# Kernel tuning notes

Measured on AMD Instinct MI355X. Metric: run time of the kernel, lower is better.

The kernel has to match this reference:

```python
import jax, jax.numpy as jnp
import numpy as np
from functools import partial

K = 1024
EMA_DECAY = 0.99
TOL = 1e-4
EPS = 1e-5
MAX_ITERS = 10


def setup_inputs() -> dict:
    key = jax.random.key(0)
    x = jax.random.normal(key, (32, 256, 1024), dtype=jnp.float32)
    return {"x": x}


def _sq_dists(xf, x_sq, centers):
    # squared euclidean distances [N, K]; argmin is identical to torch.cdist argmin
    c_sq = jnp.sum(centers * centers, axis=1)
    return x_sq[:, None] + c_sq[None, :] - 2.0 * (xf @ centers.T)


def reference(x):
    b, c, t = x.shape
    xf = jnp.transpose(x, (0, 2, 1)).reshape(-1, c)  # [N, c], N = b*t
    N = xf.shape[0]
    # _init_centers: random permutation of rows, take first K (training mode)
    perm = jax.random.permutation(jax.random.key(1), N)[:K]
    ema0 = xf[perm]  # [K, c]
    x_sq = jnp.sum(xf * xf, axis=1)  # [N]
    ones = jnp.ones((N,), dtype=xf.dtype)

    def step(carry, _):
        ema, labels_prev, done = carry
        d = _sq_dists(xf, x_sq, ema)
        labels = jnp.argmin(d, axis=1)  # [N]
        counts = jax.ops.segment_sum(ones, labels, num_segments=K)  # [K]
        sums = jax.ops.segment_sum(xf, labels, num_segments=K)      # [K, c]
        centers = sums / (counts[:, None] + EPS)
        # dead-center handling: keep old ema center where cluster is empty
        centers = jnp.where((counts == 0)[:, None], ema, centers)
        new_ema = ema * EMA_DECAY + (1.0 - EMA_DECAY) * centers
        err = jnp.linalg.norm(new_ema - centers)
        # torch loop breaks AFTER the ema update of the converged iteration;
        # once done, later iterations are no-ops.
        ema_out = jnp.where(done, ema, new_ema)
        labels_out = jnp.where(done, labels_prev, labels)
        new_done = jnp.logical_or(done, err < TOL)
        return (ema_out, labels_out, new_done), None

    init = (ema0, jnp.zeros((N,), dtype=jnp.int32), jnp.array(False))
    (ema, labels, done), _ = jax.lax.scan(step, init, None, length=MAX_ITERS)

    # if loop never broke, torch recomputes labels against final ema centers
    labels_final = jnp.argmin(_sq_dists(xf, x_sq, ema), axis=1)
    return jnp.where(done, labels, labels_final)
```

## Files before the change

kernel.cpp:

```cpp
#include <hip/hip_runtime.h>
#include <stdint.h>

#define JAX_PARTITIONABLE 1

static constexpr int C_ = 256;
static constexpr int T_ = 1024;
static constexpr int N_ = 32768;
static constexpr int K_ = 1024;
static constexpr float MARGIN_ = 0.02f;

typedef __attribute__((ext_vector_type(8))) short short8;
typedef __attribute__((ext_vector_type(4))) float f32x4;

__host__ __device__ __forceinline__ void tf2x32(uint32_t k0, uint32_t k1,
                                                uint32_t x0, uint32_t x1,
                                                uint32_t& o0, uint32_t& o1) {
  const uint32_t ks2 = k0 ^ k1 ^ 0x1BD11BDAu;
  uint32_t v0 = x0 + k0, v1 = x1 + k1;
#define TFR(d) { v0 += v1; v1 = (v1 << d) | (v1 >> (32 - d)); v1 ^= v0; }
#define TF4A TFR(13) TFR(15) TFR(26) TFR(6)
#define TF4B TFR(17) TFR(29) TFR(16) TFR(24)
  TF4A v0 += k1;  v1 += ks2 + 1u;
  TF4B v0 += ks2; v1 += k0 + 2u;
  TF4A v0 += k0;  v1 += k1 + 3u;
  TF4B v0 += k1;  v1 += ks2 + 4u;
  TF4A v0 += ks2; v1 += k0 + 5u;
  o0 = v0; o1 = v1;
#undef TFR
#undef TF4A
#undef TF4B
}

__device__ __forceinline__ uint16_t f2bf(float f) {
  const uint32_t u = __float_as_uint(f);
  return (uint16_t)((u + 0x7FFFu + ((u >> 16) & 1u)) >> 16);
}
__device__ __forceinline__ float bf2f(uint16_t h) {
  return __uint_as_float(((uint32_t)h) << 16);
}

__device__ __forceinline__ void write_bfrag(uint16_t* __restrict__ bH, uint16_t* __restrict__ bL,
                                            int k, int c, float v) {
  const int kt = k >> 4;
  const int lane = (k & 15) + (((c & 31) >> 3) << 4);
  const int ck = c >> 5;
  const int j = c & 7;
  const uint16_t h = f2bf(v);
  const uint16_t l = f2bf(v - bf2f(h));
  const size_t idx = ((((size_t)(kt << 3) + ck) << 6) + lane) * 8 + j;
  bH[idx] = h; bL[idx] = l;
}

__global__ void bits_kernel(uint32_t k0, uint32_t k1, unsigned long long* __restrict__ keys) {
#if JAX_PARTITIONABLE
  const int i = blockIdx.x * 256 + threadIdx.x;
  uint32_t o0, o1; tf2x32(k0, k1, 0u, (uint32_t)i, o0, o1);
  keys[i] = (((unsigned long long)(o0 ^ o1)) << 32) | (unsigned)i;
#else
  const int j = blockIdx.x * 256 + threadIdx.x;
  uint32_t o0, o1; tf2x32(k0, k1, (uint32_t)j, (uint32_t)(j + 16384), o0, o1);
  keys[j]         = (((unsigned long long)o0) << 32) | (unsigned)j;
  keys[j + 16384] = (((unsigned long long)o1) << 32) | (unsigned)(j + 16384);
#endif
}

__global__ void bhist_kernel(const unsigned long long* __restrict__ keys, int* __restrict__ bcnt) {
  const int i = blockIdx.x * 256 + threadIdx.x;
  atomicAdd(&bcnt[(int)(keys[i] >> 56)], 1);
}

__global__ void bscan_kernel(const int* __restrict__ bcnt, int* __restrict__ boff,
                             int* __restrict__ bcur) {
  if (threadIdx.x == 0) {
    int run = 0;
    for (int i = 0; i < 256; ++i) { boff[i] = run; bcur[i] = run; run += bcnt[i]; }
    boff[256] = run;
  }
}

__global__ void bscatter_kernel(const unsigned long long* __restrict__ keys,
                                int* __restrict__ bcur, unsigned long long* __restrict__ barr) {
  const int i = blockIdx.x * 256 + threadIdx.x;
  const unsigned long long k = keys[i];
  const int pos = atomicAdd(&bcur[(int)(k >> 56)], 1);
  barr[pos] = k;
}

template<int ROUND>
__global__ void brank_kernel(const unsigned long long* __restrict__ barr,
                             const int* __restrict__ boff,
                             int* __restrict__ val1, int* __restrict__ perm) {
  const int i = blockIdx.x * 256 + threadIdx.x;
  const unsigned long long my = barr[i];
  const int b = (int)(my >> 56);
  const int lo = boff[b], hi = boff[b + 1];
  int cnt = 0;
  #pragma unroll 4
  for (int j = lo; j < hi; ++j) cnt += (barr[j] < my) ? 1 : 0;
  const int r = lo + cnt;
  const int idx = (int)(uint32_t)my;
  if (ROUND == 1) {
    val1[r] = idx;
  } else {
    if (r < K_) perm[r] = val1[idx];
  }
}

__global__ void transpose_kernel(const float* __restrict__ x, float* __restrict__ xT) {
  __shared__ float tile[256][33];
  const int tid = threadIdx.x;
  const int b = blockIdx.x >> 5, tt = blockIdx.x & 31;
  const int t0 = tt << 5;
  const float* xb = x + (size_t)b * (C_ * T_) + t0;
  #pragma unroll
  for (int i = 0; i < 32; ++i) {
    const int idx = tid + (i << 8);
    const int c = idx >> 5, p = idx & 31;
    tile[c][p] = xb[(size_t)c * T_ + p];
  }
  __syncthreads();
  float* dst = xT + (((size_t)(b << 10) + t0) << 8);
  #pragma unroll
  for (int p = 0; p < 32; ++p)
    dst[((size_t)p << 8) + tid] = tile[tid][p];
}

__device__ __forceinline__ double block_reduce_256_f64(double v, double* red) {
  #pragma unroll
  for (int s = 1; s < 64; s <<= 1) v += __shfl_xor(v, s, 64);
  if ((threadIdx.x & 63) == 0) red[threadIdx.x >> 6] = v;
  __syncthreads();
  return red[0] + red[1] + red[2] + red[3];
}

__global__ void init_ema_kernel(const float* __restrict__ x, const int* __restrict__ perm,
                                float* __restrict__ ema, uint16_t* __restrict__ bfH,
                                uint16_t* __restrict__ bfL,
                                double* __restrict__ csq, float* __restrict__ csq32) {
  __shared__ double red[4];
  const int k = blockIdx.x, c = threadIdx.x;
  const int n = perm[k];
  const int b = n >> 10, t = n & 1023;
  const float v = x[(size_t)b * (C_ * T_) + (size_t)c * T_ + t];
  ema[((size_t)k << 8) + c] = v;
  write_bfrag(bfH, bfL, k, c, v);
  const double s = block_reduce_256_f64((double)v * (double)v, red);
  if (c == 0) { csq[k] = s; csq32[k] = (float)s; }
}

__global__ void update_kernel(float* __restrict__ ema, uint16_t* __restrict__ bfH,
                              uint16_t* __restrict__ bfL,
                              const double* __restrict__ sums4, const int* __restrict__ counts,
                              double* __restrict__ csq, float* __restrict__ csq32) {
  __shared__ double red[4];
  const int k = blockIdx.x, c = threadIdx.x;
  const size_t idx = ((size_t)k << 8) + c;
  const int cnt = counts[k];
  const float e = ema[idx];
  float center;
  if (cnt == 0) {
    center = e;
  } else {
    double sd = 0.0;
    #pragma unroll
    for (int sl = 0; sl < 4; ++sl) sd += sums4[((size_t)((sl << 10) + k) << 8) + c];
    const float s32 = (float)sd;
    const float denom = __fadd_rn((float)cnt, 1e-5f);
    center = __fdiv_rn(s32, denom);
  }
  const float ne = __fadd_rn(__fmul_rn(e, 0.99f), __fmul_rn(0.01f, center));
  ema[idx] = ne;
  write_bfrag(bfH, bfL, k, c, ne);
  const double s = block_reduce_256_f64((double)ne * (double)ne, red);
  if (c == 0) { csq[k] = s; csq32[k] = (float)s; }
}

#define AF(pl, mt, ck, lane) (((((((pl) << 2) + (mt)) << 3) + (ck)) << 6) + (lane))
__global__ __launch_bounds__(256, 2) void assign_mfma(
    const float* __restrict__ x, const short8* __restrict__ bfH, const short8* __restrict__ bfL,
    const float* __restrict__ csq32, int* __restrict__ labels,
    int* __restrict__ flagidx, int* __restrict__ flagcnt) {
  __shared__ __align__(16) char smem[81920];
  short8* afrag = (short8*)smem;
  float (*xstage)[64] = (float(*)[64])(smem + 65536);
  float* mg_d = (float*)(smem + 65536);
  float* mg_2 = mg_d + 256;
  int*   mg_k = (int*)(mg_2 + 256);

  const int tid = threadIdx.x;
  const int n0 = blockIdx.x << 6;
  const int b = n0 >> 10, t0 = n0 & 1023;
  const float* xb = x + (size_t)b * (C_ * T_) + t0;

  #pragma unroll 1
  for (int q = 0; q < 4; ++q) {
    #pragma unroll
    for (int i = 0; i < 16; ++i) {
      const int idx = tid + (i << 8);
      const int c = idx >> 6, p = idx & 63;
      xstage[c][p] = xb[(size_t)((q << 6) + c) * T_ + p];
    }
    __syncthreads();
    #pragma unroll
    for (int i = 0; i < 2; ++i) {
      const int slot = tid + (i << 8);
      const int lane = slot & 63;
      const int ckh = (slot >> 6) & 1;
      const int mt = slot >> 7;
      const int row = lane & 15;
      const int kof = (lane >> 4) << 3;
      short8 h8, l8;
      #pragma unroll
      for (int j = 0; j < 8; ++j) {
        const float v = xstage[(ckh << 5) + kof + j][(mt << 4) + row];
        const uint16_t hh = f2bf(v);
        h8[j] = (short)hh;
        l8[j] = (short)f2bf(v - bf2f(hh));
      }
      const int ck = (q << 1) + ckh;
      afrag[AF(0, mt, ck, lane)] = h8;
      afrag[AF(1, mt, ck, lane)] = l8;
    }
    __syncthreads();
  }

  const int w = tid >> 6, lane = tid & 63;

  float bd[16], b2[16]; int bk[16];
  #pragma unroll
  for (int s = 0; s < 16; ++s) { bd[s] = 3.0e38f; b2[s] = 3.0e38f; bk[s] = 0; }

  const short8* afH = afrag;
  const short8* afL = afrag + 2048;

  #pragma unroll 1
  for (int g = 0; g < 4; ++g) {
    f32x4 acc[4][4];
    #pragma unroll
    for (int mt = 0; mt < 4; ++mt)
      #pragma unroll
      for (int t = 0; t < 4; ++t) acc[mt][t] = (f32x4){0.f, 0.f, 0.f, 0.f};

    #pragma unroll 1
    for (int pass = 0; pass < 3; ++pass) {
      const short8* ap = (pass == 2) ? afL : afH;
      const short8* bp = (pass == 1) ? bfL : bfH;
      #pragma unroll 2
      for (int ck = 0; ck < 8; ++ck) {
        short8 a0 = ap[(0 << 9) + (ck << 6) + lane];
        short8 a1 = ap[(1 << 9) + (ck << 6) + lane];
        short8 a2 = ap[(2 << 9) + (ck << 6) + lane];
        short8 a3 = ap[(3 << 9) + (ck << 6) + lane];
        const size_t bbase = ((((size_t)(w << 4) + (g << 2)) << 3) + ck) * 64 + lane;
        #pragma unroll
        for (int t = 0; t < 4; ++t) {
          const short8 bf = bp[bbase + (size_t)t * 512];
          acc[0][t] = __builtin_amdgcn_mfma_f32_16x16x32_bf16(a0, bf, acc[0][t], 0, 0, 0);
          acc[1][t] = __builtin_amdgcn_mfma_f32_16x16x32_bf16(a1, bf, acc[1][t], 0, 0, 0);
          acc[2][t] = __builtin_amdgcn_mfma_f32_16x16x32_bf16(a2, bf, acc[2][t], 0, 0, 0);
          acc[3][t] = __builtin_amdgcn_mfma_f32_16x16x32_bf16(a3, bf, acc[3][t], 0, 0, 0);
        }
      }
    }
    #pragma unroll
    for (int t = 0; t < 4; ++t) {
      const int kt = (w << 4) + (g << 2) + t;
      const int k = (kt << 4) + (lane & 15);
      const float cq = csq32[k];
      #pragma unroll
      for (int mt = 0; mt < 4; ++mt)
        #pragma unroll
        for (int r = 0; r < 4; ++r) {
          const float d = cq - 2.0f * acc[mt][t][r];
          const int s = (mt << 2) + r;
          if (d < bd[s]) { b2[s] = bd[s]; bd[s] = d; bk[s] = k; }
          else if (d < b2[s]) b2[s] = d;
        }
    }
  }

  #pragma unroll
  for (int s = 0; s < 16; ++s) {
    #pragma unroll
    for (int sh = 1; sh < 16; sh <<= 1) {
      const float od = __shfl_xor(bd[s], sh, 64);
      const float o2 = __shfl_xor(b2[s], sh, 64);
      const int   ok = __shfl_xor(bk[s], sh, 64);
      if (od < bd[s] || (od == bd[s] && ok < bk[s])) {
        b2[s] = fminf(o2, bd[s]); bd[s] = od; bk[s] = ok;
      } else {
        b2[s] = fminf(b2[s], od);
      }
    }
  }
  if ((lane & 15) == 0) {
    #pragma unroll
    for (int s = 0; s < 16; ++s) {
      const int mt = s >> 2, r = s & 3;
      const int pt = (mt << 4) + ((lane >> 4) << 2) + r;
      mg_d[(w << 6) + pt] = bd[s]; mg_2[(w << 6) + pt] = b2[s]; mg_k[(w << 6) + pt] = bk[s];
    }
  }
  __syncthreads();

  if (tid < 64) {
    float fb = mg_d[tid], f2 = mg_2[tid]; int fk = mg_k[tid];
    #pragma unroll
    for (int ww = 1; ww < 4; ++ww) {
      const float od = mg_d[(ww << 6) + tid], o2 = mg_2[(ww << 6) + tid];
      const int ok = mg_k[(ww << 6) + tid];
      if (od < fb) { f2 = fminf(fb, o2); fb = od; fk = ok; }
      else f2 = fminf(f2, fminf(od, o2));
    }
    const int n = n0 + tid;
    labels[n] = fk;
    if (f2 - fb <= MARGIN_) { const int p = atomicAdd(flagcnt, 1); flagidx[p] = n; }
  }
}

__global__ void refine_kernel(const float* __restrict__ x, const float* __restrict__ ema,
                              const double* __restrict__ csq,
                              const int* __restrict__ flagidx, const int* __restrict__ flagcnt,
                              int* __restrict__ labels) {
  __shared__ float xr[C_];
  __shared__ double rd[4]; __shared__ int rk[4];
  const int tid = threadIdx.x;
  const int cnt = *flagcnt;
  for (int it = blockIdx.x; it < cnt; it += gridDim.x) {
    const int n = flagidx[it];
    const int b = n >> 10, t = n & 1023;
    xr[tid] = x[(size_t)b * (C_ * T_) + (size_t)tid * T_ + t];
    __syncthreads();
    double bdv = 1e300; int bkv = 0;
    #pragma unroll 1
    for (int r = 0; r < 4; ++r) {
      const int k = (r << 8) + tid;
      const float* er = ema + ((size_t)k << 8);
      double acc = 0.0;
      #pragma unroll 4
      for (int c4 = 0; c4 < 64; ++c4) {
        const float4 ev = *(const float4*)(er + (c4 << 2));
        const float4 xv = *(const float4*)(&xr[c4 << 2]);
        acc = fma((double)xv.x, (double)ev.x, acc);
        acc = fma((double)xv.y, (double)ev.y, acc);
        acc = fma((double)xv.z, (double)ev.z, acc);
        acc = fma((double)xv.w, (double)ev.w, acc);
      }
      const double d = csq[k] - 2.0 * acc;
      if (d < bdv) { bdv = d; bkv = k; }
    }
    #pragma unroll
    for (int s = 1; s < 64; s <<= 1) {
      const double od = __shfl_xor(bdv, s, 64);
      const int    ok = __shfl_xor(bkv, s, 64);
      if (od < bdv || (od == bdv && ok < bkv)) { bdv = od; bkv = ok; }
    }
    if ((tid & 63) == 0) { rd[tid >> 6] = bdv; rk[tid >> 6] = bkv; }
    __syncthreads();
    if (tid == 0) {
      #pragma unroll
      for (int wv = 1; wv < 4; ++wv)
        if (rd[wv] < bdv || (rd[wv] == bdv && rk[wv] < bkv)) { bdv = rd[wv]; bkv = rk[wv]; }
      if (bkv != labels[n]) labels[n] = bkv;
    }
    __syncthreads();
  }
}

__global__ void hist_kernel(const int* __restrict__ labels, int* __restrict__ counts) {
  const int n = blockIdx.x * 256 + threadIdx.x;
  atomicAdd(&counts[labels[n]], 1);
}

__global__ void prefix_kernel(const int* __restrict__ counts, int* __restrict__ offsets,
                              int* __restrict__ cursor) {
  __shared__ int wsum[4];
  const int tid = threadIdx.x;
  const int lane = tid & 63, w = tid >> 6;
  const int c0 = counts[(tid << 2)], c1 = counts[(tid << 2) + 1];
  const int c2 = counts[(tid << 2) + 2], c3 = counts[(tid << 2) + 3];
  const int s = c0 + c1 + c2 + c3;
  int inc = s;
  #pragma unroll
  for (int sh = 1; sh < 64; sh <<= 1) {
    const int t = __shfl_up(inc, sh, 64);
    if (lane >= sh) inc += t;
  }
  if (lane == 63) wsum[w] = inc;
  __syncthreads();
  int wof = 0;
  #pragma unroll
  for (int i = 0; i < 4; ++i) if (i < w) wof += wsum[i];
  int run = wof + inc - s;
  offsets[(tid << 2)] = run;     cursor[(tid << 2)] = run;     run += c0;
  offsets[(tid << 2) + 1] = run; cursor[(tid << 2) + 1] = run; run += c1;
  offsets[(tid << 2) + 2] = run; cursor[(tid << 2) + 2] = run; run += c2;
  offsets[(tid << 2) + 3] = run; cursor[(tid << 2) + 3] = run;
}

__global__ void scatter_sorted_kernel(const int* __restrict__ labels, int* __restrict__ cursor,
                                      int* __restrict__ sortedIdx) {
  const int n = blockIdx.x * 256 + threadIdx.x;
  const int pos = atomicAdd(&cursor[labels[n]], 1);
  sortedIdx[pos] = n;
}

template<int TRANS>
__global__ void segsum_kernel(const float* __restrict__ x, const float* __restrict__ xT,
                              const int* __restrict__ sortedIdx, const int* __restrict__ offsets,
                              const int* __restrict__ counts, double* __restrict__ sums4) {
  const int k = blockIdx.x >> 2, sl = blockIdx.x & 3;
  const int tid = threadIdx.x;
  const int cnt = counts[k], off = offsets[k];
  const int i0 = (cnt * sl) >> 2, i1 = (cnt * (sl + 1)) >> 2;
  double acc = 0.0;
  int i = i0;
  for (; i + 4 <= i1; i += 4) {
    float v0, v1, v2, v3;
    if (TRANS) {
      const int na = sortedIdx[off + i],     nb = sortedIdx[off + i + 1];
      const int nc = sortedIdx[off + i + 2], nd = sortedIdx[off + i + 3];
      v0 = xT[((size_t)na << 8) + tid]; v1 = xT[((size_t)nb << 8) + tid];
      v2 = xT[((size_t)nc << 8) + tid]; v3 = xT[((size_t)nd << 8) + tid];
    } else {
      const int na = sortedIdx[off + i],     nb = sortedIdx[off + i + 1];
      const int nc = sortedIdx[off + i + 2], nd = sortedIdx[off + i + 3];
      v0 = x[(size_t)(na >> 10) * (C_ * T_) + (size_t)tid * T_ + (na & 1023)];
      v1 = x[(size_t)(nb >> 10) * (C_ * T_) + (size_t)tid * T_ + (nb & 1023)];
      v2 = x[(size_t)(nc >> 10) * (C_ * T_) + (size_t)tid * T_ + (nc & 1023)];
      v3 = x[(size_t)(nd >> 10) * (C_ * T_) + (size_t)tid * T_ + (nd & 1023)];
    }
    acc += (double)v0; acc += (double)v1; acc += (double)v2; acc += (double)v3;
  }
  for (; i < i1; ++i) {
    const int n = sortedIdx[off + i];
    const float v = TRANS ? xT[((size_t)n << 8) + tid]
                          : x[(size_t)(n >> 10) * (C_ * T_) + (size_t)tid * T_ + (n & 1023)];
    acc += (double)v;
  }
  sums4[((size_t)((sl << 10) + k) << 8) + tid] = acc;
}

extern "C" void kernel_launch(void* const* d_in, const int* in_sizes, int n_in,
                              void* d_out, int out_size, void* d_ws, size_t ws_size,
                              hipStream_t stream) {
  const float* x = (const float*)d_in[0];
  int* out = (int*)d_out;
  char* ws = (char*)d_ws;

  float*    ema   = (float*)   (ws + 0);
  uint16_t* bfH   = (uint16_t*)(ws + 1048576);
  uint16_t* bfL   = (uint16_t*)(ws + 1572864);
  double*   sums4 = (double*)  (ws + 2097152);
  unsigned long long* keys = (unsigned long long*)(ws + 2097152);
  unsigned long long* barr = (unsigned long long*)(ws + 2097152 + 262144);
  int*    val1   = (int*)  (ws + 2097152 + 524288);
  const size_t MISC = 2097152 + 8388608;
  int*    counts  = (int*)  (ws + MISC);
  int*    flagcnt = (int*)  (ws + MISC + 4096);
  int*    offsets = (int*)  (ws + MISC + 8192);
  int*    cursor  = (int*)  (ws + MISC + 12288);
  double* csq     = (double*)(ws + MISC + 16384);
  float*  csq32   = (float*) (ws + MISC + 24576);
  int*    perm    = (int*)  (ws + MISC + 28672);
  int*    flagidx = (int*)  (ws + MISC + 32768);
  int*    sortedIdx = (int*)(ws + MISC + 163840);
  int*    bcnt    = (int*)  (ws + MISC + 294912);
  int*    boff    = (int*)  (ws + MISC + 295936);
  int*    bcur    = (int*)  (ws + MISC + 297984);
  const size_t XT_OFF = 11534336;
  float*  xT      = (float*) (ws + XT_OFF);
  const bool trans_ok = ws_size >= XT_OFF + (size_t)N_ * C_ * 4;

  uint32_t s1h, s1l, s2h, s2l;
  {
#if JAX_PARTITIONABLE
    uint32_t ch, cl;
    tf2x32(0u, 1u, 0u, 0u, ch, cl);
    tf2x32(0u, 1u, 0u, 1u, s1h, s1l);
    tf2x32(ch, cl, 0u, 1u, s2h, s2l);
#else
    uint32_t a0, a1, b0, b1, ch, cl;
    tf2x32(0u, 1u, 0u, 2u, a0, a1); tf2x32(0u, 1u, 1u, 3u, b0, b1);
    ch = a0; cl = b0; s1h = a1; s1l = b1;
    tf2x32(ch, cl, 0u, 2u, a0, a1); tf2x32(ch, cl, 1u, 3u, b0, b1);
    s2h = a1; s2l = b1;
#endif
  }

#if JAX_PARTITIONABLE
  bits_kernel<<<128, 256, 0, stream>>>(s1h, s1l, keys);
#else
  bits_kernel<<<64, 256, 0, stream>>>(s1h, s1l, keys);
#endif
  hipMemsetAsync(bcnt, 0, 1024, stream);
  bhist_kernel<<<128, 256, 0, stream>>>(keys, bcnt);
  bscan_kernel<<<1, 64, 0, stream>>>(bcnt, boff, bcur);
  bscatter_kernel<<<128, 256, 0, stream>>>(keys, bcur, barr);
  brank_kernel<1><<<128, 256, 0, stream>>>(barr, boff, val1, perm);

#if JAX_PARTITIONABLE
  bits_kernel<<<128, 256, 0, stream>>>(s2h, s2l, keys);
#else
  bits_kernel<<<64, 256, 0, stream>>>(s2h, s2l, keys);
#endif
  hipMemsetAsync(bcnt, 0, 1024, stream);
  bhist_kernel<<<128, 256, 0, stream>>>(keys, bcnt);
  bscan_kernel<<<1, 64, 0, stream>>>(bcnt, boff, bcur);
  bscatter_kernel<<<128, 256, 0, stream>>>(keys, bcur, barr);
  brank_kernel<2><<<128, 256, 0, stream>>>(barr, boff, val1, perm);

  init_ema_kernel<<<K_, 256, 0, stream>>>(x, perm, ema, bfH, bfL, csq, csq32);
  if (trans_ok) transpose_kernel<<<1024, 256, 0, stream>>>(x, xT);

  for (int it = 0; it < 10; ++it) {
    hipMemsetAsync(counts, 0, 8192, stream);
    assign_mfma<<<512, 256, 0, stream>>>(x, (const short8*)bfH, (const short8*)bfL,
                                         csq32, out, flagidx, flagcnt);
    refine_kernel<<<512, 256, 0, stream>>>(x, ema, csq, flagidx, flagcnt, out);
    hist_kernel<<<128, 256, 0, stream>>>(out, counts);
    prefix_kernel<<<1, 256, 0, stream>>>(counts, offsets, cursor);
    scatter_sorted_kernel<<<128, 256, 0, stream>>>(out, cursor, sortedIdx);
    if (trans_ok)
      segsum_kernel<1><<<4096, 256, 0, stream>>>(x, xT, sortedIdx, offsets, counts, sums4);
    else
      segsum_kernel<0><<<4096, 256, 0, stream>>>(x, xT, sortedIdx, offsets, counts, sums4);
    update_kernel<<<K_, 256, 0, stream>>>(ema, bfH, bfL, sums4, counts, csq, csq32);
  }
  hipMemsetAsync(flagcnt, 0, 4, stream);
  assign_mfma<<<512, 256, 0, stream>>>(x, (const short8*)bfH, (const short8*)bfL,
                                       csq32, out, flagidx, flagcnt);
  refine_kernel<<<512, 256, 0, stream>>>(x, ema, csq, flagidx, flagcnt, out);
}
```

Baseline: 3.073 ms.

## Halve assign tile, software-pipeline B fragment loads, fuse histogram into assign/refine

The assign kernel now handles 32 points per block instead of 64. That halves LDS use and lets launch bounds target 3 blocks per CU over twice as many blocks. The three bf16-split passes are flattened into a single 24-step loop that double-buffers the center fragment loads from global memory ahead of the MFMAs, to hide load latency. The separate histogram kernel is removed: assign counts labels atomically, and refine adjusts counts when it relabels a point. The cost is that each block reuses the center fragments for fewer points, so total global B-fragment traffic doubles, and atomic contention on counts rises.

```diff
diff --git a/kernel.cpp b/kernel.cpp
--- a/kernel.cpp
+++ b/kernel.cpp
@@ -175,38 +175,46 @@
   if (c == 0) { csq[k] = s; csq32[k] = (float)s; }
 }
 
-#define AF(pl, mt, ck, lane) (((((((pl) << 2) + (mt)) << 3) + (ck)) << 6) + (lane))
-__global__ __launch_bounds__(256, 2) void assign_mfma(
+#define AF2(pl, mt, ck, lane) (((((((pl) << 1) + (mt)) << 3) + (ck)) << 6) + (lane))
+#define LOADB(m, dst) { \
+  const int _p = (m) >> 3, _c = (m) & 7; \
+  const short8* _bp = (_p == 1) ? bfL : bfH; \
+  const size_t _a = base0 + ((size_t)_c << 6); \
+  dst[0] = _bp[_a]; dst[1] = _bp[_a + 512]; dst[2] = _bp[_a + 1024]; dst[3] = _bp[_a + 1536]; }
+#define LOADA(m, A0, A1) { \
+  const int _p = (m) >> 3, _c = (m) & 7; \
+  const short8* _ap = (_p == 2) ? afL : afH; \
+  A0 = _ap[(_c << 6) + lane]; A1 = _ap[512 + (_c << 6) + lane]; }
+
+__global__ __launch_bounds__(256, 3) void assign_mfma(
     const float* __restrict__ x, const short8* __restrict__ bfH, const short8* __restrict__ bfL,
     const float* __restrict__ csq32, int* __restrict__ labels,
-    int* __restrict__ flagidx, int* __restrict__ flagcnt) {
-  __shared__ __align__(16) char smem[81920];
+    int* __restrict__ flagidx, int* __restrict__ flagcnt, int* __restrict__ counts) {
+  __shared__ __align__(16) char smem[40960];
   short8* afrag = (short8*)smem;
-  float (*xstage)[64] = (float(*)[64])(smem + 65536);
-  float* mg_d = (float*)(smem + 65536);
-  float* mg_2 = mg_d + 256;
-  int*   mg_k = (int*)(mg_2 + 256);
+  float (*xstage)[32] = (float(*)[32])(smem + 32768);
+  float* mg_d = (float*)(smem + 32768);
+  float* mg_2 = mg_d + 128;
+  int*   mg_k = (int*)(mg_2 + 128);
 
   const int tid = threadIdx.x;
-  const int n0 = blockIdx.x << 6;
+  const int n0 = blockIdx.x << 5;
   const int b = n0 >> 10, t0 = n0 & 1023;
   const float* xb = x + (size_t)b * (C_ * T_) + t0;
 
   #pragma unroll 1
   for (int q = 0; q < 4; ++q) {
     #pragma unroll
-    for (int i = 0; i < 16; ++i) {
+    for (int i = 0; i < 8; ++i) {
       const int idx = tid + (i << 8);
-      const int c = idx >> 6, p = idx & 63;
+      const int c = idx >> 5, p = idx & 31;
       xstage[c][p] = xb[(size_t)((q << 6) + c) * T_ + p];
     }
     __syncthreads();
-    #pragma unroll
-    for (int i = 0; i < 2; ++i) {
-      const int slot = tid + (i << 8);
-      const int lane = slot & 63;
-      const int ckh = (slot >> 6) & 1;
-      const int mt = slot >> 7;
+    {
+      const int lane = tid & 63;
+      const int ckh = (tid >> 6) & 1;
+      const int mt = tid >> 7;
       const int row = lane & 15;
       const int kof = (lane >> 4) << 3;
       short8 h8, l8;
@@ -218,57 +226,61 @@
         l8[j] = (short)f2bf(v - bf2f(hh));
       }
       const int ck = (q << 1) + ckh;
-      afrag[AF(0, mt, ck, lane)] = h8;
-      afrag[AF(1, mt, ck, lane)] = l8;
+      afrag[AF2(0, mt, ck, lane)] = h8;
+      afrag[AF2(1, mt, ck, lane)] = l8;
     }
     __syncthreads();
   }
 
   const int w = tid >> 6, lane = tid & 63;
-
-  float bd[16], b2[16]; int bk[16];
-  #pragma unroll
-  for (int s = 0; s < 16; ++s) { bd[s] = 3.0e38f; b2[s] = 3.0e38f; bk[s] = 0; }
-
   const short8* afH = afrag;
-  const short8* afL = afrag + 2048;
+  const short8* afL = afrag + 1024;
+
+  float bd[8], b2[8]; int bk[8];
+  #pragma unroll
+  for (int s = 0; s < 8; ++s) { bd[s] = 3.0e38f; b2[s] = 3.0e38f; bk[s] = 0; }
 
   #pragma unroll 1
   for (int g = 0; g < 4; ++g) {
-    f32x4 acc[4][4];
-    #pragma unroll
-    for (int mt = 0; mt < 4; ++mt)
+    const size_t base0 = ((size_t)((w << 4) + (g << 2)) << 9) + lane;
+    f32x4 acc[2][4];
+    #pragma unroll
+    for (int mt = 0; mt < 2; ++mt)
       #pragma unroll
       for (int t = 0; t < 4; ++t) acc[mt][t] = (f32x4){0.f, 0.f, 0.f, 0.f};
 
+    short8 bufA[4], bufB[4], a0, a1;
+    LOADB(0, bufA);
+    LOADB(1, bufB);
     #pragma unroll 1
-    for (int pass = 0; pass < 3; ++pass) {
-      const short8* ap = (pass == 2) ? afL : afH;
-      const short8* bp = (pass == 1) ? bfL : bfH;
-      #pragma unroll 2
-      for (int ck = 0; ck < 8; ++ck) {
-        short8 a0 = ap[(0 << 9) + (ck << 6) + lane];
-        short8 a1 = ap[(1 << 9) + (ck << 6) + lane];
-        short8 a2 = ap[(2 << 9) + (ck << 6) + lane];
-        short8 a3 = ap[(3 << 9) + (ck << 6) + lane];
-        const size_t bbase = ((((size_t)(w << 4) + (g << 2)) << 3) + ck) * 64 + lane;
-        #pragma unroll
-        for (int t = 0; t < 4; ++t) {
-          const short8 bf = bp[bbase + (size_t)t * 512];
-          acc[0][t] = __builtin_amdgcn_mfma_f32_16x16x32_bf16(a0, bf, acc[0][t], 0, 0, 0);
-          acc[1][t] = __builtin_amdgcn_mfma_f32_16x16x32_bf16(a1, bf, acc[1][t], 0, 0, 0);
-          acc[2][t] = __builtin_amdgcn_mfma_f32_16x16x32_bf16(a2, bf, acc[2][t], 0, 0, 0);
-          acc[3][t] = __builtin_amdgcn_mfma_f32_16x16x32_bf16(a3, bf, acc[3][t], 0, 0, 0);
-        }
+    for (int mm = 0; mm < 12; ++mm) {
+      const int m0 = mm << 1;
+      short8 nb0[4], nb1[4];
+      if (mm < 11) LOADB(m0 + 2, nb0);
+      LOADA(m0, a0, a1);
+      #pragma unroll
+      for (int t = 0; t < 4; ++t) {
+        acc[0][t] = __builtin_amdgcn_mfma_f32_16x16x32_bf16(a0, bufA[t], acc[0][t], 0, 0, 0);
+        acc[1][t] = __builtin_amdgcn_mfma_f32_16x16x32_bf16(a1, bufA[t], acc[1][t], 0, 0, 0);
       }
-    }
+      if (mm < 11) { bufA[0] = nb0[0]; bufA[1] = nb0[1]; bufA[2] = nb0[2]; bufA[3] = nb0[3]; }
+      if (mm < 11) LOADB(m0 + 3, nb1);
+      LOADA(m0 + 1, a0, a1);
+      #pragma unroll
+      for (int t = 0; t < 4; ++t) {
+        acc[0][t] = __builtin_amdgcn_mfma_f32_16x16x32_bf16(a0, bufB[t], acc[0][t], 0, 0, 0);
+        acc[1][t] = __builtin_amdgcn_mfma_f32_16x16x32_bf16(a1, bufB[t], acc[1][t], 0, 0, 0);
+      }
+      if (mm < 11) { bufB[0] = nb1[0]; bufB[1] = nb1[1]; bufB[2] = nb1[2]; bufB[3] = nb1[3]; }
+    }
+
     #pragma unroll
     for (int t = 0; t < 4; ++t) {
       const int kt = (w << 4) + (g << 2) + t;
       const int k = (kt << 4) + (lane & 15);
       const float cq = csq32[k];
       #pragma unroll
-      for (int mt = 0; mt < 4; ++mt)
+      for (int mt = 0; mt < 2; ++mt)
         #pragma unroll
         for (int r = 0; r < 4; ++r) {
           const float d = cq - 2.0f * acc[mt][t][r];
@@ -280,7 +292,7 @@
   }
 
   #pragma unroll
-  for (int s = 0; s < 16; ++s) {
+  for (int s = 0; s < 8; ++s) {
     #pragma unroll
     for (int sh = 1; sh < 16; sh <<= 1) {
       const float od = __shfl_xor(bd[s], sh, 64);
@@ -295,25 +307,26 @@
   }
   if ((lane & 15) == 0) {
     #pragma unroll
-    for (int s = 0; s < 16; ++s) {
+    for (int s = 0; s < 8; ++s) {
       const int mt = s >> 2, r = s & 3;
       const int pt = (mt << 4) + ((lane >> 4) << 2) + r;
-      mg_d[(w << 6) + pt] = bd[s]; mg_2[(w << 6) + pt] = b2[s]; mg_k[(w << 6) + pt] = bk[s];
+      mg_d[(w << 5) + pt] = bd[s]; mg_2[(w << 5) + pt] = b2[s]; mg_k[(w << 5) + pt] = bk[s];
     }
   }
   __syncthreads();
 
-  if (tid < 64) {
+  if (tid < 32) {
     float fb = mg_d[tid], f2 = mg_2[tid]; int fk = mg_k[tid];
     #pragma unroll
     for (int ww = 1; ww < 4; ++ww) {
-      const float od = mg_d[(ww << 6) + tid], o2 = mg_2[(ww << 6) + tid];
-      const int ok = mg_k[(ww << 6) + tid];
+      const float od = mg_d[(ww << 5) + tid], o2 = mg_2[(ww << 5) + tid];
+      const int ok = mg_k[(ww << 5) + tid];
       if (od < fb) { f2 = fminf(fb, o2); fb = od; fk = ok; }
       else f2 = fminf(f2, fminf(od, o2));
     }
     const int n = n0 + tid;
     labels[n] = fk;
+    atomicAdd(&counts[fk], 1);
     if (f2 - fb <= MARGIN_) { const int p = atomicAdd(flagcnt, 1); flagidx[p] = n; }
   }
 }
@@ -321,7 +334,7 @@
 __global__ void refine_kernel(const float* __restrict__ x, const float* __restrict__ ema,
                               const double* __restrict__ csq,
                               const int* __restrict__ flagidx, const int* __restrict__ flagcnt,
-                              int* __restrict__ labels) {
+                              int* __restrict__ labels, int* __restrict__ counts) {
   __shared__ float xr[C_];
   __shared__ double rd[4]; __shared__ int rk[4];
   const int tid = threadIdx.x;
@@ -361,15 +374,14 @@
       #pragma unroll
       for (int wv = 1; wv < 4; ++wv)
         if (rd[wv] < bdv || (rd[wv] == bdv && rk[wv] < bkv)) { bdv = rd[wv]; bkv = rk[wv]; }
-      if (bkv != labels[n]) labels[n] = bkv;
+      const int old = labels[n];
+      if (bkv != old) {
+        labels[n] = bkv;
+        if (counts != nullptr) { atomicAdd(&counts[old], -1); atomicAdd(&counts[bkv], 1); }
+      }
     }
     __syncthreads();
   }
-}
-
-__global__ void hist_kernel(const int* __restrict__ labels, int* __restrict__ counts) {
-  const int n = blockIdx.x * 256 + threadIdx.x;
-  atomicAdd(&counts[labels[n]], 1);
 }
 
 __global__ void prefix_kernel(const int* __restrict__ counts, int* __restrict__ offsets,
@@ -515,10 +527,9 @@
 
   for (int it = 0; it < 10; ++it) {
     hipMemsetAsync(counts, 0, 8192, stream);
-    assign_mfma<<<512, 256, 0, stream>>>(x, (const short8*)bfH, (const short8*)bfL,
-                                         csq32, out, flagidx, flagcnt);
-    refine_kernel<<<512, 256, 0, stream>>>(x, ema, csq, flagidx, flagcnt, out);
-    hist_kernel<<<128, 256, 0, stream>>>(out, counts);
+    assign_mfma<<<1024, 256, 0, stream>>>(x, (const short8*)bfH, (const short8*)bfL,
+                                          csq32, out, flagidx, flagcnt, counts);
+    refine_kernel<<<512, 256, 0, stream>>>(x, ema, csq, flagidx, flagcnt, out, counts);
     prefix_kernel<<<1, 256, 0, stream>>>(counts, offsets, cursor);
     scatter_sorted_kernel<<<128, 256, 0, stream>>>(out, cursor, sortedIdx);
     if (trans_ok)
@@ -527,8 +538,8 @@
       segsum_kernel<0><<<4096, 256, 0, stream>>>(x, xT, sortedIdx, offsets, counts, sums4);
     update_kernel<<<K_, 256, 0, stream>>>(ema, bfH, bfL, sums4, counts, csq, csq32);
   }
-  hipMemsetAsync(flagcnt, 0, 4, stream);
-  assign_mfma<<<512, 256, 0, stream>>>(x, (const short8*)bfH, (const short8*)bfL,
-                                       csq32, out, flagidx, flagcnt);
-  refine_kernel<<<512, 256, 0, stream>>>(x, ema, csq, flagidx, flagcnt, out);
-}
+  hipMemsetAsync(counts, 0, 8192, stream);
+  assign_mfma<<<1024, 256, 0, stream>>>(x, (const short8*)bfH, (const short8*)bfL,
+                                        csq32, out, flagidx, flagcnt, counts);
+  refine_kernel<<<512, 256, 0, stream>>>(x, ema, csq, flagidx, flagcnt, out, nullptr);
+}
```

Result: faster. 2.734 ms (-11.0%).
